# Kernel tuning notes

Measured on AMD Instinct MI355X. Metric: run time of the kernel, lower is better.

Reference implementation:

```python
import jax, jax.numpy as jnp
import numpy as np

IN, ENC, H = 60, 32, 64  # input feat, encoder out, LSTM hidden per direction


def _lstm_scan(x_tbf, W_ih, W_hh, b):
    """x_tbf: [T,B,ENC]. Returns final (h, c), each [B,H]. PyTorch gate order i,f,g,o."""
    B = x_tbf.shape[1]
    h0 = jnp.zeros((B, H), x_tbf.dtype)
    c0 = jnp.zeros((B, H), x_tbf.dtype)

    def step(carry, x_t):
        h, c = carry
        gates = x_t @ W_ih.T + h @ W_hh.T + b  # [B, 4H]
        i, f, g, o = jnp.split(gates, 4, axis=-1)
        c = jax.nn.sigmoid(f) * c + jax.nn.sigmoid(i) * jnp.tanh(g)
        h = jax.nn.sigmoid(o) * jnp.tanh(c)
        return (h, c), None

    (h_fin, c_fin), _ = jax.lax.scan(step, (h0, c0), x_tbf)
    return h_fin, c_fin


def setup_inputs() -> dict:
    key = jax.random.key(0)
    ks = jax.random.split(key, 10)
    B, T = 256, 4096
    s_enc = 1.0 / np.sqrt(IN)
    s_lstm = 1.0 / np.sqrt(H)
    s_fin = 1.0 / np.sqrt(2 * H)
    return {
        "c": jax.random.normal(ks[0], (B, T, IN), jnp.float32),
        "W_enc": jax.random.uniform(ks[1], (ENC, IN), jnp.float32, -s_enc, s_enc),
        "b_enc": jax.random.uniform(ks[2], (ENC,), jnp.float32, -s_enc, s_enc),
        "W_ih_f": jax.random.uniform(ks[3], (4 * H, ENC), jnp.float32, -s_lstm, s_lstm),
        "W_hh_f": jax.random.uniform(ks[4], (4 * H, H), jnp.float32, -s_lstm, s_lstm),
        "b_f": jax.random.uniform(ks[5], (4 * H,), jnp.float32, -s_lstm, s_lstm),
        "W_ih_b": jax.random.uniform(ks[6], (4 * H, ENC), jnp.float32, -s_lstm, s_lstm),
        "W_hh_b": jax.random.uniform(ks[7], (4 * H, H), jnp.float32, -s_lstm, s_lstm),
        "b_b": jax.random.uniform(ks[8], (4 * H,), jnp.float32, -s_lstm, s_lstm),
        "W_fin": jax.random.uniform(ks[9], (3, 2 * H), jnp.float32, -s_fin, s_fin),
        "b_fin": jnp.zeros((3,), jnp.float32),
    }


def reference(c, W_enc, b_enc, W_ih_f, W_hh_f, b_f, W_ih_b, W_hh_b, b_b, W_fin, b_fin):
    # SequenceWise linear encoder: [B,T,60] -> [B,T,32]
    x = c @ W_enc.T + b_enc
    x_tbf = jnp.transpose(x, (1, 0, 2))  # [T,B,ENC]
    # Bidirectional LSTM; original code unpacks (h_n, c_n) as (c, h),
    # so it feeds the final CELL states into final_fc — reproduce that.
    _, c_fwd = _lstm_scan(x_tbf, W_ih_f, W_hh_f, b_f)
    _, c_bwd = _lstm_scan(x_tbf[::-1], W_ih_b, W_hh_b, b_b)
    hidden = jnp.concatenate([c_fwd, c_bwd], axis=1)  # [B, 2H]
    return hidden @ W_fin.T + b_fin  # [B, 3]
```

## Files before the change

### kernel.cpp

```cpp
#include <hip/hip_runtime.h>
#include <hip/hip_bf16.h>

#define T_LEN 4096

typedef __attribute__((ext_vector_type(8))) short bfrag8;
typedef __attribute__((ext_vector_type(4))) float f32x4;

__device__ __forceinline__ void wg_barrier() {
  asm volatile("s_waitcnt lgkmcnt(0)\ns_barrier" ::: "memory");
}

__device__ __forceinline__ float fact(float x, float S, float A, float B) {
  float e = __builtin_amdgcn_exp2f(S * x);
  return A + B * __builtin_amdgcn_rcpf(1.0f + e);
}
__device__ __forceinline__ float ftanh(float x) {
  float e = __builtin_amdgcn_exp2f(2.8853900817779268f * x);
  return 1.0f - 2.0f * __builtin_amdgcn_rcpf(1.0f + e);
}
template <int SEL>
__device__ __forceinline__ float qb(float v) {
  union { float f; int i; } u;
  u.f = v;
  u.i = __builtin_amdgcn_mov_dpp(u.i, SEL * 0x55, 0xF, 0xF, true);
  return u.f;
}

__global__ void prep_enc(const float* __restrict__ W_enc,
                         __hip_bfloat16* __restrict__ Wencb) {
  int u = threadIdx.x;
  if (u < 32) {
    for (int k = 0; k < 64; ++k)
      Wencb[u * 64 + k] = __float2bfloat16(k < 60 ? W_enc[u * 60 + k] : 0.0f);
  }
}

__global__ __launch_bounds__(256) void encoder(const float* __restrict__ c,
                                               const __hip_bfloat16* __restrict__ Wencb,
                                               __hip_bfloat16* __restrict__ x) {
  const int lane = threadIdx.x & 63, wave = threadIdx.x >> 6;
  const int q = lane >> 4, l15 = lane & 15;
  const size_t r0 = ((size_t)blockIdx.x * 4 + wave) * 16;

  bfrag8 bf00 = *(const bfrag8*)(Wencb + (0 * 16 + l15) * 64 + 0 * 32 + q * 8);
  bfrag8 bf01 = *(const bfrag8*)(Wencb + (0 * 16 + l15) * 64 + 1 * 32 + q * 8);
  bfrag8 bf10 = *(const bfrag8*)(Wencb + (1 * 16 + l15) * 64 + 0 * 32 + q * 8);
  bfrag8 bf11 = *(const bfrag8*)(Wencb + (1 * 16 + l15) * 64 + 1 * 32 + q * 8);

  const float* cr = c + (r0 + l15) * 60;
  float4 a0 = *(const float4*)(cr + q * 8);
  float4 a1 = *(const float4*)(cr + q * 8 + 4);
  float4 a2 = *(const float4*)(cr + 32 + q * 8);
  float4 a3 = (q == 3) ? float4{0.f, 0.f, 0.f, 0.f}
                       : *(const float4*)(cr + 36 + q * 8);
  union { bfrag8 v; __hip_bfloat16 h[8]; } A0, A1;
  A0.h[0] = __float2bfloat16(a0.x); A0.h[1] = __float2bfloat16(a0.y);
  A0.h[2] = __float2bfloat16(a0.z); A0.h[3] = __float2bfloat16(a0.w);
  A0.h[4] = __float2bfloat16(a1.x); A0.h[5] = __float2bfloat16(a1.y);
  A0.h[6] = __float2bfloat16(a1.z); A0.h[7] = __float2bfloat16(a1.w);
  A1.h[0] = __float2bfloat16(a2.x); A1.h[1] = __float2bfloat16(a2.y);
  A1.h[2] = __float2bfloat16(a2.z); A1.h[3] = __float2bfloat16(a2.w);
  A1.h[4] = __float2bfloat16(a3.x); A1.h[5] = __float2bfloat16(a3.y);
  A1.h[6] = __float2bfloat16(a3.z); A1.h[7] = __float2bfloat16(a3.w);

  f32x4 acc0 = {0.f, 0.f, 0.f, 0.f}, acc1 = {0.f, 0.f, 0.f, 0.f};
  acc0 = __builtin_amdgcn_mfma_f32_16x16x32_bf16(A0.v, bf00, acc0, 0, 0, 0);
  acc1 = __builtin_amdgcn_mfma_f32_16x16x32_bf16(A0.v, bf10, acc1, 0, 0, 0);
  acc0 = __builtin_amdgcn_mfma_f32_16x16x32_bf16(A1.v, bf01, acc0, 0, 0, 0);
  acc1 = __builtin_amdgcn_mfma_f32_16x16x32_bf16(A1.v, bf11, acc1, 0, 0, 0);

#pragma unroll
  for (int r = 0; r < 4; ++r) {
    size_t row = r0 + q * 4 + r;
    x[row * 32 + l15]      = __float2bfloat16(acc0[r]);
    x[row * 32 + 16 + l15] = __float2bfloat16(acc1[r]);
  }
}

__global__ void prep_weights(const float* __restrict__ b_enc,
                             const float* __restrict__ W_ih_f,
                             const float* __restrict__ W_hh_f,
                             const float* __restrict__ b_f,
                             const float* __restrict__ W_ih_b,
                             const float* __restrict__ W_hh_b,
                             const float* __restrict__ b_b,
                             __hip_bfloat16* __restrict__ Wc,
                             float* __restrict__ biasc) {
  const int dir = blockIdx.x;
  const int np = threadIdx.x;
  const int w = np >> 6, tile = (np >> 4) & 3, cc = np & 15;
  const int unit = w * 16 + tile * 4 + (cc >> 2);
  const int gate = cc & 3;
  const int no = gate * 64 + unit;
  const float* W_ih = dir ? W_ih_b : W_ih_f;
  const float* W_hh = dir ? W_hh_b : W_hh_f;
  const float* bv = dir ? b_b : b_f;
  __hip_bfloat16* row = Wc + (size_t)(dir * 256 + np) * 96;
#pragma unroll
  for (int k = 0; k < 32; ++k) row[k] = __float2bfloat16(W_ih[no * 32 + k]);
#pragma unroll
  for (int j = 0; j < 64; ++j) row[32 + j] = __float2bfloat16(W_hh[no * 64 + j]);
  float bb = bv[no];
#pragma unroll
  for (int e = 0; e < 32; ++e) bb += W_ih[no * 32 + e] * b_enc[e];
  biasc[dir * 256 + np] = bb;
}

__global__ __launch_bounds__(256, 2) void lstm_main(
    const __hip_bfloat16* __restrict__ x, const __hip_bfloat16* __restrict__ Wc,
    const float* __restrict__ biasc, float* __restrict__ cfin) {
  __shared__ short Hbuf[2][64];

  const int tid = threadIdx.x, lane = tid & 63, wave = tid >> 6;
  const int quad = lane >> 4, l15 = lane & 15;
  const int g = lane & 3;
  const int unit = wave * 16 + quad * 4 + (l15 >> 2);
  const int dir = (int)blockIdx.x & 1;
  const int b = (int)blockIdx.x >> 1;

  bfrag8 wf[4][3];
  float bias[4];
#pragma unroll
  for (int tl = 0; tl < 4; ++tl) {
    const int np = wave * 64 + tl * 16 + l15;
    const __hip_bfloat16* wr = Wc + (size_t)(dir * 256 + np) * 96 + quad * 8;
#pragma unroll
    for (int kt = 0; kt < 3; ++kt) wf[tl][kt] = *(const bfrag8*)(wr + kt * 32);
    bias[tl] = biasc[dir * 256 + np];
  }

  const bool isg = (g == 2);
  const float S = isg ? 2.8853900817779268f : -1.4426950408889634f;
  const float Aa = isg ? 1.0f : 0.0f;
  const float Bb = isg ? -2.0f : 1.0f;

  const __hip_bfloat16* xr = x + (size_t)b * T_LEN * 32 + quad * 8;

  if (tid < 128) ((short*)Hbuf)[tid] = 0;

  bfrag8 xb[4];
#pragma unroll
  for (int qq = 0; qq < 4; ++qq) {
    int tp = dir ? (T_LEN - 1 - qq) : qq;
    xb[qq] = *(const bfrag8*)(xr + (size_t)tp * 32);
  }

  float cst = 0.f;
  wg_barrier();

#pragma unroll 4
  for (int t = 0; t < T_LEN; ++t) {
    const int cur = t & 1;
    bfrag8 ahA = *(const bfrag8*)&Hbuf[cur][quad * 8];
    bfrag8 ahB = *(const bfrag8*)&Hbuf[cur][32 + quad * 8];
    f32x4 ax0 = {bias[0], bias[0], bias[0], bias[0]};
    f32x4 ax1 = {bias[1], bias[1], bias[1], bias[1]};
    f32x4 ax2 = {bias[2], bias[2], bias[2], bias[2]};
    f32x4 ax3 = {bias[3], bias[3], bias[3], bias[3]};
    ax0 = __builtin_amdgcn_mfma_f32_16x16x32_bf16(xb[t & 3], wf[0][0], ax0, 0, 0, 0);
    ax1 = __builtin_amdgcn_mfma_f32_16x16x32_bf16(xb[t & 3], wf[1][0], ax1, 0, 0, 0);
    ax2 = __builtin_amdgcn_mfma_f32_16x16x32_bf16(xb[t & 3], wf[2][0], ax2, 0, 0, 0);
    ax3 = __builtin_amdgcn_mfma_f32_16x16x32_bf16(xb[t & 3], wf[3][0], ax3, 0, 0, 0);
    f32x4 ah0 = {0.f, 0.f, 0.f, 0.f}, ah1 = {0.f, 0.f, 0.f, 0.f};
    f32x4 ah2 = {0.f, 0.f, 0.f, 0.f}, ah3 = {0.f, 0.f, 0.f, 0.f};
    ah0 = __builtin_amdgcn_mfma_f32_16x16x32_bf16(ahA, wf[0][1], ah0, 0, 0, 0);
    ah1 = __builtin_amdgcn_mfma_f32_16x16x32_bf16(ahA, wf[1][1], ah1, 0, 0, 0);
    ah2 = __builtin_amdgcn_mfma_f32_16x16x32_bf16(ahA, wf[2][1], ah2, 0, 0, 0);
    ah3 = __builtin_amdgcn_mfma_f32_16x16x32_bf16(ahA, wf[3][1], ah3, 0, 0, 0);
    ah0 = __builtin_amdgcn_mfma_f32_16x16x32_bf16(ahB, wf[0][2], ah0, 0, 0, 0);
    ah1 = __builtin_amdgcn_mfma_f32_16x16x32_bf16(ahB, wf[1][2], ah1, 0, 0, 0);
    ah2 = __builtin_amdgcn_mfma_f32_16x16x32_bf16(ahB, wf[2][2], ah2, 0, 0, 0);
    ah3 = __builtin_amdgcn_mfma_f32_16x16x32_bf16(ahB, wf[3][2], ah3, 0, 0, 0);
    {
      int tn = t + 4; if (tn > T_LEN - 1) tn = T_LEN - 1;
      int tp = dir ? (T_LEN - 1 - tn) : tn;
      xb[t & 3] = *(const bfrag8*)(xr + (size_t)tp * 32);
    }
    float vx01 = (quad & 1) ? ax1[0] : ax0[0];
    float vx23 = (quad & 1) ? ax3[0] : ax2[0];
    float vx = (quad & 2) ? vx23 : vx01;
    float vh01 = (quad & 1) ? ah1[0] : ah0[0];
    float vh23 = (quad & 1) ? ah3[0] : ah2[0];
    float vh = (quad & 2) ? vh23 : vh01;
    float a = fact(vx + vh, S, Aa, Bb);
    float gi = qb<0>(a), gf = qb<1>(a), gg = qb<2>(a), go = qb<3>(a);
    cst = gf * cst + gi * gg;
    float h = go * ftanh(cst);
    if (g == 0) *(__hip_bfloat16*)&Hbuf[cur ^ 1][unit] = __float2bfloat16(h);
    wg_barrier();
  }

  if (g == 0) {
    cfin[(size_t)(dir * 256 + b) * 64 + unit] = cst;
  }
}

__global__ void final_fc(const float* __restrict__ cfin,
                         const float* __restrict__ W_fin,
                         const float* __restrict__ b_fin,
                         float* __restrict__ out) {
  int b = threadIdx.x;
  const float* cf = cfin + (size_t)b * 64;
  const float* cb = cfin + (size_t)(256 + b) * 64;
  float a0 = b_fin[0], a1 = b_fin[1], a2 = b_fin[2];
  for (int u = 0; u < 64; ++u) {
    float vf = cf[u], vb = cb[u];
    a0 += W_fin[0 * 128 + u] * vf + W_fin[0 * 128 + 64 + u] * vb;
    a1 += W_fin[1 * 128 + u] * vf + W_fin[1 * 128 + 64 + u] * vb;
    a2 += W_fin[2 * 128 + u] * vf + W_fin[2 * 128 + 64 + u] * vb;
  }
  out[b * 3 + 0] = a0;
  out[b * 3 + 1] = a1;
  out[b * 3 + 2] = a2;
}

extern "C" void kernel_launch(void* const* d_in, const int* in_sizes, int n_in,
                              void* d_out, int out_size, void* d_ws, size_t ws_size,
                              hipStream_t stream) {
  (void)in_sizes; (void)n_in; (void)out_size; (void)ws_size;
  const float* c      = (const float*)d_in[0];
  const float* W_enc  = (const float*)d_in[1];
  const float* b_enc  = (const float*)d_in[2];
  const float* W_ih_f = (const float*)d_in[3];
  const float* W_hh_f = (const float*)d_in[4];
  const float* b_f    = (const float*)d_in[5];
  const float* W_ih_b = (const float*)d_in[6];
  const float* W_hh_b = (const float*)d_in[7];
  const float* b_b    = (const float*)d_in[8];
  const float* W_fin  = (const float*)d_in[9];
  const float* b_fin  = (const float*)d_in[10];
  float* out = (float*)d_out;

  char* ws = (char*)d_ws;
  __hip_bfloat16* x     = (__hip_bfloat16*)ws;
  __hip_bfloat16* Wc    = (__hip_bfloat16*)(ws + 67108864);
  float* biasc          = (float*)(ws + 67108864 + 98304);
  __hip_bfloat16* Wencb = (__hip_bfloat16*)(ws + 67108864 + 100352);
  float* cfin           = (float*)(ws + 67108864 + 104448);

  prep_enc<<<1, 32, 0, stream>>>(W_enc, Wencb);
  prep_weights<<<2, 256, 0, stream>>>(b_enc, W_ih_f, W_hh_f, b_f,
                                      W_ih_b, W_hh_b, b_b, Wc, biasc);
  encoder<<<16384, 256, 0, stream>>>(c, Wencb, x);
  lstm_main<<<512, 256, 0, stream>>>(x, Wc, biasc, cfin);
  final_fc<<<1, 256, 0, stream>>>(cfin, W_fin, b_fin, out);
}
```

Baseline: 1.576 ms.

## Process two batch rows per LSTM workgroup using spare MFMA rows

Each workgroup now advances two batch elements through the recurrence. It uses otherwise-wasted rows of the 16x16 MFMA tile: odd lanes load x and h for the second batch row. The grid is halved to 256 blocks, and the hidden buffer gains a per-batch slot with padding. This roughly halves the number of serial step-loops per CU at the cost of a few more activation ops per step, but it also halves the number of concurrent blocks on a 256-CU part.

```diff
diff --git a/kernel.cpp b/kernel.cpp
--- a/kernel.cpp
+++ b/kernel.cpp
@@ -109,14 +109,16 @@
 __global__ __launch_bounds__(256, 2) void lstm_main(
     const __hip_bfloat16* __restrict__ x, const __hip_bfloat16* __restrict__ Wc,
     const float* __restrict__ biasc, float* __restrict__ cfin) {
-  __shared__ short Hbuf[2][64];
+  __shared__ __align__(16) short Hbuf[2][2][72];
 
   const int tid = threadIdx.x, lane = tid & 63, wave = tid >> 6;
   const int quad = lane >> 4, l15 = lane & 15;
   const int g = lane & 3;
   const int unit = wave * 16 + quad * 4 + (l15 >> 2);
   const int dir = (int)blockIdx.x & 1;
-  const int b = (int)blockIdx.x >> 1;
+  const int pair = (int)blockIdx.x >> 1;
+  const int b0 = pair * 2;
+  const int bl = b0 + (l15 & 1);
 
   bfrag8 wf[4][3];
   float bias[4];
@@ -134,9 +136,10 @@
   const float Aa = isg ? 1.0f : 0.0f;
   const float Bb = isg ? -2.0f : 1.0f;
 
-  const __hip_bfloat16* xr = x + (size_t)b * T_LEN * 32 + quad * 8;
-
-  if (tid < 128) ((short*)Hbuf)[tid] = 0;
+  const __hip_bfloat16* xr = x + (size_t)bl * T_LEN * 32 + quad * 8;
+
+  ((short*)Hbuf)[tid] = 0;
+  if (tid < 32) ((short*)Hbuf)[256 + tid] = 0;
 
   bfrag8 xb[4];
 #pragma unroll
@@ -145,14 +148,15 @@
     xb[qq] = *(const bfrag8*)(xr + (size_t)tp * 32);
   }
 
-  float cst = 0.f;
+  float cst0 = 0.f, cst1 = 0.f;
   wg_barrier();
 
 #pragma unroll 4
   for (int t = 0; t < T_LEN; ++t) {
     const int cur = t & 1;
-    bfrag8 ahA = *(const bfrag8*)&Hbuf[cur][quad * 8];
-    bfrag8 ahB = *(const bfrag8*)&Hbuf[cur][32 + quad * 8];
+    const short* hb = &Hbuf[cur][l15 & 1][0];
+    bfrag8 ahA = *(const bfrag8*)(hb + quad * 8);
+    bfrag8 ahB = *(const bfrag8*)(hb + 32 + quad * 8);
     f32x4 ax0 = {bias[0], bias[0], bias[0], bias[0]};
     f32x4 ax1 = {bias[1], bias[1], bias[1], bias[1]};
     f32x4 ax2 = {bias[2], bias[2], bias[2], bias[2]};
@@ -176,23 +180,35 @@
       int tp = dir ? (T_LEN - 1 - tn) : tn;
       xb[t & 3] = *(const bfrag8*)(xr + (size_t)tp * 32);
     }
-    float vx01 = (quad & 1) ? ax1[0] : ax0[0];
-    float vx23 = (quad & 1) ? ax3[0] : ax2[0];
-    float vx = (quad & 2) ? vx23 : vx01;
-    float vh01 = (quad & 1) ? ah1[0] : ah0[0];
-    float vh23 = (quad & 1) ? ah3[0] : ah2[0];
-    float vh = (quad & 2) ? vh23 : vh01;
-    float a = fact(vx + vh, S, Aa, Bb);
-    float gi = qb<0>(a), gf = qb<1>(a), gg = qb<2>(a), go = qb<3>(a);
-    cst = gf * cst + gi * gg;
-    float h = go * ftanh(cst);
-    if (g == 0) *(__hip_bfloat16*)&Hbuf[cur ^ 1][unit] = __float2bfloat16(h);
+    float vx0a = (quad & 1) ? ax1[0] : ax0[0];
+    float vx0b = (quad & 1) ? ax3[0] : ax2[0];
+    float vx0 = (quad & 2) ? vx0b : vx0a;
+    float vh0a = (quad & 1) ? ah1[0] : ah0[0];
+    float vh0b = (quad & 1) ? ah3[0] : ah2[0];
+    float vh0 = (quad & 2) ? vh0b : vh0a;
+    float vx1a = (quad & 1) ? ax1[1] : ax0[1];
+    float vx1b = (quad & 1) ? ax3[1] : ax2[1];
+    float vx1 = (quad & 2) ? vx1b : vx1a;
+    float vh1a = (quad & 1) ? ah1[1] : ah0[1];
+    float vh1b = (quad & 1) ? ah3[1] : ah2[1];
+    float vh1 = (quad & 2) ? vh1b : vh1a;
+    float a0 = fact(vx0 + vh0, S, Aa, Bb);
+    float a1 = fact(vx1 + vh1, S, Aa, Bb);
+    float gi0 = qb<0>(a0), gf0 = qb<1>(a0), gg0 = qb<2>(a0), go0 = qb<3>(a0);
+    float gi1 = qb<0>(a1), gf1 = qb<1>(a1), gg1 = qb<2>(a1), go1 = qb<3>(a1);
+    cst0 = gf0 * cst0 + gi0 * gg0;
+    cst1 = gf1 * cst1 + gi1 * gg1;
+    float h0 = go0 * ftanh(cst0);
+    float h1 = go1 * ftanh(cst1);
+    if (g < 2) {
+      float hv = g ? h1 : h0;
+      *(__hip_bfloat16*)&Hbuf[cur ^ 1][g][unit] = __float2bfloat16(hv);
+    }
     wg_barrier();
   }
 
-  if (g == 0) {
-    cfin[(size_t)(dir * 256 + b) * 64 + unit] = cst;
-  }
+  if (g == 0) cfin[(size_t)(dir * 256 + b0) * 64 + unit] = cst0;
+  if (g == 1) cfin[(size_t)(dir * 256 + b0 + 1) * 64 + unit] = cst1;
 }
 
 __global__ void final_fc(const float* __restrict__ cfin,
@@ -242,6 +258,6 @@
   prep_weights<<<2, 256, 0, stream>>>(b_enc, W_ih_f, W_hh_f, b_f,
                                       W_ih_b, W_hh_b, b_b, Wc, biasc);
   encoder<<<16384, 256, 0, stream>>>(c, Wencb, x);
-  lstm_main<<<512, 256, 0, stream>>>(x, Wc, biasc, cfin);
+  lstm_main<<<256, 256, 0, stream>>>(x, Wc, biasc, cfin);
   final_fc<<<1, 256, 0, stream>>>(cfin, W_fin, b_fin, out);
 }
```

Result: faster. 1.509 ms (-4.2%).
